# Kernel tuning notes

Hardware: AMD Instinct MI355X
Metric: run time of the kernel (lower is better)

Reference implementation:

```python
import jax, jax.numpy as jnp
import numpy as np

N, E, D, H = 50000, 800000, 128, 8
DH = D // H
EPS = 1e-12


def setup_inputs() -> dict:
    key = jax.random.key(0)
    ks = jax.random.split(key, 12)
    s = 0.02
    return {
        "h": jax.random.normal(ks[0], (N, D), jnp.float32),
        "Wq": jax.random.normal(ks[1], (D, D), jnp.float32) * s,
        "bq": jax.random.normal(ks[2], (D,), jnp.float32) * s,
        "Wk": jax.random.normal(ks[3], (D, D), jnp.float32) * s,
        "bk": jax.random.normal(ks[4], (D,), jnp.float32) * s,
        "Wv": jax.random.normal(ks[5], (D, D), jnp.float32) * s,
        "bv": jax.random.normal(ks[6], (D,), jnp.float32) * s,
        "Wo": jax.random.normal(ks[7], (D, D), jnp.float32) * s,
        "bo": jax.random.normal(ks[8], (D,), jnp.float32) * s,
        "gamma": jnp.ones((D,), jnp.float32),
        "beta": jnp.zeros((D,), jnp.float32),
        "src": jax.random.randint(ks[9], (E,), 0, N, jnp.int32),
        "dst": jax.random.randint(ks[10], (E,), 0, N, jnp.int32),
    }


def reference(h, Wq, bq, Wk, bk, Wv, bv, Wo, bo, gamma, beta, src, dst):
    n = h.shape[0]
    # node-wise projections, split into heads: [N, H, DH]
    Q = (h @ Wq + bq).reshape(n, H, DH)
    K = (h @ Wk + bk).reshape(n, H, DH)
    V = (h @ Wv + bv).reshape(n, H, DH)
    # edge-wise scores: sum over head dim of K[src] * Q[dst] -> [E, H]
    scores = jnp.sum(K[src] * Q[dst], axis=-1)
    # edge softmax, normalized over incoming edges of each dst node
    m = jax.lax.stop_gradient(jax.ops.segment_max(scores, dst, num_segments=n))
    ex = jnp.exp(scores - m[dst])
    denom = jax.ops.segment_sum(ex, dst, num_segments=n)
    p = ex / denom[dst]  # [E, H]
    # weighted message + scatter-sum aggregate -> [N, H, DH]
    msg = V[src] * p[:, :, None]
    agg = jax.ops.segment_sum(msg, dst, num_segments=n).reshape(n, D)
    # BertSelfOutput: dense + residual + layernorm (dropout is identity in eval)
    y = agg @ Wo + bo + h
    mu = jnp.mean(y, axis=-1, keepdims=True)
    var = jnp.mean(jnp.square(y - mu), axis=-1, keepdims=True)
    out = (y - mu) / jnp.sqrt(var + EPS) * gamma + beta
    return out
```

## Files before the change

### kernel.cpp

```cpp
#include <hip/hip_runtime.h>
#include <hip/hip_bf16.h>
#include <math.h>

#define D 128
#define EPS 1e-12f
#define CPAD 16

typedef __attribute__((ext_vector_type(8))) short bf16x8;
typedef __attribute__((ext_vector_type(4))) float f32x4;
typedef __attribute__((ext_vector_type(2))) float f32x2;

__device__ __forceinline__ unsigned short f2bf(float f) {
    unsigned int u = __float_as_uint(f);
    return (unsigned short)((u + 0x7fffu + ((u >> 16) & 1u)) >> 16);
}
__device__ __forceinline__ float bf2f_lo(unsigned int packed) {
    return __uint_as_float(packed << 16);
}
__device__ __forceinline__ float bf2f_hi(unsigned int packed) {
    return __uint_as_float(packed & 0xffff0000u);
}
__device__ __forceinline__ unsigned char f2fp8(float f) {
    return (unsigned char)__builtin_amdgcn_cvt_pk_fp8_f32(f, f, 0, false);
}

__global__ __launch_bounds__(256) void prep_kernel(
    const float* __restrict__ Wq, const float* __restrict__ Wk,
    const float* __restrict__ Wv, const float* __restrict__ Wo,
    unsigned short* __restrict__ WT,
    const int* __restrict__ dst, int* __restrict__ counts,
    int* __restrict__ ticket, int E) {
    int bx = blockIdx.x;
    int tid = threadIdx.x;
    if (bx < 64) {
        __shared__ unsigned short tile[32][33];
        int m = bx >> 4;
        int t = bx & 15;
        const float* W = (m == 0) ? Wq : (m == 1) ? Wk : (m == 2) ? Wv : Wo;
        int r0 = (t & 3) * 32;
        int c0 = (t >> 2) * 32;
        int row = tid >> 3, c4 = (tid & 7) * 4;
        float4 v = *(const float4*)&W[(size_t)(r0 + row) * D + c0 + c4];
        tile[c4 + 0][row] = f2bf(v.x);
        tile[c4 + 1][row] = f2bf(v.y);
        tile[c4 + 2][row] = f2bf(v.z);
        tile[c4 + 3][row] = f2bf(v.w);
        __syncthreads();
        unsigned int lo = (unsigned int)tile[row][c4] | ((unsigned int)tile[row][c4 + 1] << 16);
        unsigned int hi = (unsigned int)tile[row][c4 + 2] | ((unsigned int)tile[row][c4 + 3] << 16);
        uint2 pk; pk.x = lo; pk.y = hi;
        int n = c0 + row;
        int ct = n >> 4, l15 = n & 15;
        int ks = t & 3;
        int quad = c4 >> 3;
        int j = c4 & 7;
        size_t off = (size_t)m * 16384 + (size_t)(((ct * 4 + ks) * 64) + quad * 16 + l15) * 8 + j;
        *(uint2*)&WT[off] = pk;
    } else {
        int e = ((bx - 64) * 256 + tid) * 4;
        if (e >= E) return;
        if (e + 3 < E) {
            int4 d4 = *(const int4*)&dst[e];
            int4 t4;
            t4.x = atomicAdd(&counts[d4.x * CPAD], 1);
            t4.y = atomicAdd(&counts[d4.y * CPAD], 1);
            t4.z = atomicAdd(&counts[d4.z * CPAD], 1);
            t4.w = atomicAdd(&counts[d4.w * CPAD], 1);
            *(int4*)&ticket[e] = t4;
        } else {
            for (int i = e; i < E; ++i) ticket[i] = atomicAdd(&counts[dst[i] * CPAD], 1);
        }
    }
}

__device__ __forceinline__ int block_incl_scan256(int v, int tid, int* wsum) {
    int lane = tid & 63;
    int wid = tid >> 6;
#pragma unroll
    for (int off = 1; off < 64; off <<= 1) {
        int t = __shfl_up(v, off, 64);
        if (lane >= off) v += t;
    }
    if (lane == 63) wsum[wid] = v;
    __syncthreads();
#pragma unroll
    for (int w = 0; w < 4; ++w)
        if (w < wid) v += wsum[w];
    return v;
}

__global__ void scan1_kernel(const int* __restrict__ counts, int* __restrict__ offsets,
                             int* __restrict__ chunksum, int n) {
    __shared__ int wsum[4];
    int tid = threadIdx.x;
    int i = blockIdx.x * 256 + tid;
    int v = (i < n) ? counts[i * CPAD] : 0;
    int incl = block_incl_scan256(v, tid, wsum);
    if (i < n) offsets[i + 1] = incl;
    if (tid == 255) chunksum[blockIdx.x] = incl;
}

__global__ void scan23_kernel(int* __restrict__ offsets, const int* __restrict__ chunksum, int n) {
    __shared__ int wsum[4];
    int bx = blockIdx.x, tid = threadIdx.x;
    int v = 0;
    for (int t = tid; t < bx; t += 256) v += chunksum[t];
#pragma unroll
    for (int off = 32; off >= 1; off >>= 1) v += __shfl_xor(v, off, 64);
    if ((tid & 63) == 0) wsum[tid >> 6] = v;
    __syncthreads();
    int base = wsum[0] + wsum[1] + wsum[2] + wsum[3];
    int i = bx * 256 + tid;
    if (i < n) {
        offsets[i + 1] += base;
        if (i == 0) offsets[0] = 0;
    }
}

__global__ __launch_bounds__(256) void fill_qkv_kernel(
    const int* __restrict__ dst, const int* __restrict__ src,
    const int* __restrict__ ticket, const int* __restrict__ offsets,
    int* __restrict__ psrc, int E, int e4blocks,
    const float* __restrict__ h, const unsigned short* __restrict__ WT,
    const float* __restrict__ bq, const float* __restrict__ bk, const float* __restrict__ bv,
    unsigned short* __restrict__ Qb, unsigned char* __restrict__ KV8, int n) {
    __shared__ __align__(16) unsigned short wt[16384];
    int bx = blockIdx.x;
    int tid = threadIdx.x;
    if (bx < e4blocks) {
        int e = (bx * 256 + tid) * 4;
        if (e >= E) return;
        if (e + 3 < E) {
            int4 d4 = *(const int4*)&dst[e];
            int4 s4 = *(const int4*)&src[e];
            int4 t4 = *(const int4*)&ticket[e];
            psrc[offsets[d4.x] + t4.x] = s4.x;
            psrc[offsets[d4.y] + t4.y] = s4.y;
            psrc[offsets[d4.z] + t4.z] = s4.z;
            psrc[offsets[d4.w] + t4.w] = s4.w;
        } else {
            for (int i = e; i < E; ++i) psrc[offsets[dst[i]] + ticket[i]] = src[i];
        }
        return;
    }
    int bid = bx - e4blocks;
    int lane = tid & 63, wave = tid >> 6;
    int quad = lane >> 4, l15 = lane & 15;
    int rt = bid * 64 + wave * 16;

    int rowA = min(rt + l15, n - 1);
    bf16x8 af[4];
#pragma unroll
    for (int ks = 0; ks < 4; ++ks) {
        const float* ap = &h[(size_t)rowA * D + ks * 32 + quad * 8];
        float4 a0 = *(const float4*)ap;
        float4 a1 = *(const float4*)(ap + 4);
        union { unsigned short u[8]; bf16x8 v; } pk;
        pk.u[0] = f2bf(a0.x); pk.u[1] = f2bf(a0.y);
        pk.u[2] = f2bf(a0.z); pk.u[3] = f2bf(a0.w);
        pk.u[4] = f2bf(a1.x); pk.u[5] = f2bf(a1.y);
        pk.u[6] = f2bf(a1.z); pk.u[7] = f2bf(a1.w);
        af[ks] = pk.v;
    }

    for (int m = 0; m < 3; ++m) {
#pragma unroll
        for (int it = 0; it < 8; ++it) {
            int idx = it * 256 + tid;
            *(uint4*)&wt[idx * 8] = *(const uint4*)&WT[(size_t)m * 16384 + idx * 8];
        }
        __syncthreads();

        f32x4 acc[8];
#pragma unroll
        for (int ct = 0; ct < 8; ++ct) {
            acc[ct] = (f32x4){0.f, 0.f, 0.f, 0.f};
#pragma unroll
            for (int ks = 0; ks < 4; ++ks) {
                bf16x8 bfr = *(const bf16x8*)&wt[((ct * 4 + ks) * 64 + lane) * 8];
                acc[ct] = __builtin_amdgcn_mfma_f32_16x16x32_bf16(af[ks], bfr, acc[ct], 0, 0, 0);
            }
        }
        __syncthreads();

        const float* bias = (m == 0) ? bq : (m == 1) ? bk : bv;
#pragma unroll
        for (int ct = 0; ct < 8; ++ct) {
            int col = ct * 16 + l15;
            float bb = bias[col];
#pragma unroll
            for (int r = 0; r < 4; ++r) {
                int row = rt + quad * 4 + r;
                if (row < n) {
                    float v = acc[ct][r] + bb;
                    if (m == 0)      Qb[(size_t)row * D + col] = f2bf(v);
                    else if (m == 1) KV8[(size_t)row * 256 + col] = f2fp8(v);
                    else             KV8[(size_t)row * 256 + 128 + col] = f2fp8(v);
                }
            }
        }
    }
}

__global__ __launch_bounds__(256) void edge_attn_kernel(
    const unsigned short* __restrict__ Qb, const unsigned char* __restrict__ KV8,
    const int* __restrict__ offsets, const int* __restrict__ psrc,
    unsigned short* __restrict__ aggb, int n) {
    int node = (blockIdx.x * 256 + threadIdx.x) >> 5;
    int l32 = threadIdx.x & 31;
    if (node >= n) return;
    int start = offsets[node], end = offsets[node + 1];
    int j = l32 >> 3, hd = l32 & 7;

    const unsigned short* qp = &Qb[(size_t)node * D + hd * 16];
    uint4 qa = *(const uint4*)qp;
    uint4 qb = *(const uint4*)(qp + 8);
    float q[16];
    q[0] = bf2f_lo(qa.x);  q[1] = bf2f_hi(qa.x);
    q[2] = bf2f_lo(qa.y);  q[3] = bf2f_hi(qa.y);
    q[4] = bf2f_lo(qa.z);  q[5] = bf2f_hi(qa.z);
    q[6] = bf2f_lo(qa.w);  q[7] = bf2f_hi(qa.w);
    q[8] = bf2f_lo(qb.x);  q[9] = bf2f_hi(qb.x);
    q[10] = bf2f_lo(qb.y); q[11] = bf2f_hi(qb.y);
    q[12] = bf2f_lo(qb.z); q[13] = bf2f_hi(qb.z);
    q[14] = bf2f_lo(qb.w); q[15] = bf2f_hi(qb.w);

    float l = 0.f;
    float acc[16] = {};

    if (start < end) {
        int s0 = psrc[min(start + j, end - 1)];
        int s1 = (start + 4 < end) ? psrc[min(start + 4 + j, end - 1)] : 0;
        const unsigned char* kvp = &KV8[(size_t)s0 * 256 + hd * 16];
        uint4 ku = *(const uint4*)kvp;
        uint4 vu = *(const uint4*)(kvp + 128);
        for (int base = start; base < end; base += 4) {
            const unsigned char* kvpn = &KV8[(size_t)s1 * 256 + hd * 16];
            uint4 kun = *(const uint4*)kvpn;
            uint4 vun = *(const uint4*)(kvpn + 128);
            int s2 = (base + 8 < end) ? psrc[min(base + 8 + j, end - 1)] : 0;
            bool valid = (base + j) < end;

            float kf[16], vf[16];
            {
                f32x2 t;
                t = __builtin_amdgcn_cvt_pk_f32_fp8(ku.x, false); kf[0] = t.x;  kf[1] = t.y;
                t = __builtin_amdgcn_cvt_pk_f32_fp8(ku.x, true);  kf[2] = t.x;  kf[3] = t.y;
                t = __builtin_amdgcn_cvt_pk_f32_fp8(ku.y, false); kf[4] = t.x;  kf[5] = t.y;
                t = __builtin_amdgcn_cvt_pk_f32_fp8(ku.y, true);  kf[6] = t.x;  kf[7] = t.y;
                t = __builtin_amdgcn_cvt_pk_f32_fp8(ku.z, false); kf[8] = t.x;  kf[9] = t.y;
                t = __builtin_amdgcn_cvt_pk_f32_fp8(ku.z, true);  kf[10] = t.x; kf[11] = t.y;
                t = __builtin_amdgcn_cvt_pk_f32_fp8(ku.w, false); kf[12] = t.x; kf[13] = t.y;
                t = __builtin_amdgcn_cvt_pk_f32_fp8(ku.w, true);  kf[14] = t.x; kf[15] = t.y;
                t = __builtin_amdgcn_cvt_pk_f32_fp8(vu.x, false); vf[0] = t.x;  vf[1] = t.y;
                t = __builtin_amdgcn_cvt_pk_f32_fp8(vu.x, true);  vf[2] = t.x;  vf[3] = t.y;
                t = __builtin_amdgcn_cvt_pk_f32_fp8(vu.y, false); vf[4] = t.x;  vf[5] = t.y;
                t = __builtin_amdgcn_cvt_pk_f32_fp8(vu.y, true);  vf[6] = t.x;  vf[7] = t.y;
                t = __builtin_amdgcn_cvt_pk_f32_fp8(vu.z, false); vf[8] = t.x;  vf[9] = t.y;
                t = __builtin_amdgcn_cvt_pk_f32_fp8(vu.z, true);  vf[10] = t.x; vf[11] = t.y;
                t = __builtin_amdgcn_cvt_pk_f32_fp8(vu.w, false); vf[12] = t.x; vf[13] = t.y;
                t = __builtin_amdgcn_cvt_pk_f32_fp8(vu.w, true);  vf[14] = t.x; vf[15] = t.y;
            }

            float sc = q[0] * kf[0];
#pragma unroll
            for (int i = 1; i < 16; ++i) sc = fmaf(q[i], kf[i], sc);

            float p = valid ? __expf(sc) : 0.f;
            l += p;
#pragma unroll
            for (int i = 0; i < 16; ++i) acc[i] = fmaf(p, vf[i], acc[i]);
            ku = kun; vu = vun; s1 = s2;
        }
    }

#pragma unroll
    for (int off = 8; off <= 16; off <<= 1) {
        l += __shfl_xor(l, off, 64);
#pragma unroll
        for (int i = 0; i < 16; ++i) acc[i] += __shfl_xor(acc[i], off, 64);
    }
    float inv = (l > 0.f) ? 1.f / l : 0.f;
    if (j == 0) {
        uint4 o0, o1;
        o0.x = (unsigned int)f2bf(acc[0] * inv) | ((unsigned int)f2bf(acc[1] * inv) << 16);
        o0.y = (unsigned int)f2bf(acc[2] * inv) | ((unsigned int)f2bf(acc[3] * inv) << 16);
        o0.z = (unsigned int)f2bf(acc[4] * inv) | ((unsigned int)f2bf(acc[5] * inv) << 16);
        o0.w = (unsigned int)f2bf(acc[6] * inv) | ((unsigned int)f2bf(acc[7] * inv) << 16);
        o1.x = (unsigned int)f2bf(acc[8] * inv) | ((unsigned int)f2bf(acc[9] * inv) << 16);
        o1.y = (unsigned int)f2bf(acc[10] * inv) | ((unsigned int)f2bf(acc[11] * inv) << 16);
        o1.z = (unsigned int)f2bf(acc[12] * inv) | ((unsigned int)f2bf(acc[13] * inv) << 16);
        o1.w = (unsigned int)f2bf(acc[14] * inv) | ((unsigned int)f2bf(acc[15] * inv) << 16);
        unsigned short* op = &aggb[(size_t)node * D + hd * 16];
        *(uint4*)op = o0;
        *(uint4*)(op + 8) = o1;
    }
}

__global__ __launch_bounds__(256) void out_ln_mfma_kernel(
    const unsigned short* __restrict__ aggb, const unsigned short* __restrict__ WTo,
    const float* __restrict__ bo, const float* __restrict__ hres,
    const float* __restrict__ gamma, const float* __restrict__ beta,
    float* __restrict__ out, int n) {
    int tid = threadIdx.x;
    int lane = tid & 63, wave = tid >> 6;
    int quad = lane >> 4, l15 = lane & 15;
    int rt = blockIdx.x * 64 + wave * 16;

    int rowA = min(rt + l15, n - 1);
    bf16x8 af[4];
#pragma unroll
    for (int ks = 0; ks < 4; ++ks)
        af[ks] = *(const bf16x8*)&aggb[(size_t)rowA * D + ks * 32 + quad * 8];

    f32x4 acc[8];
#pragma unroll
    for (int ct = 0; ct < 8; ++ct) {
        acc[ct] = (f32x4){0.f, 0.f, 0.f, 0.f};
#pragma unroll
        for (int ks = 0; ks < 4; ++ks) {
            bf16x8 bfr = *(const bf16x8*)&WTo[(size_t)((ct * 4 + ks) * 64 + lane) * 8];
            acc[ct] = __builtin_amdgcn_mfma_f32_16x16x32_bf16(af[ks], bfr, acc[ct], 0, 0, 0);
        }
    }

    float bb[8], gg[8], be[8];
#pragma unroll
    for (int ct = 0; ct < 8; ++ct) {
        int col = ct * 16 + l15;
        bb[ct] = bo[col];
        gg[ct] = gamma[col];
        be[ct] = beta[col];
    }
#pragma unroll
    for (int ct = 0; ct < 8; ++ct) {
        int col = ct * 16 + l15;
#pragma unroll
        for (int r = 0; r < 4; ++r) {
            int row = rt + quad * 4 + r;
            float hv = (row < n) ? hres[(size_t)row * D + col] : 0.f;
            acc[ct][r] = acc[ct][r] + bb[ct] + hv;
        }
    }

#pragma unroll
    for (int r = 0; r < 4; ++r) {
        float s1 = 0.f, s2 = 0.f;
#pragma unroll
        for (int ct = 0; ct < 8; ++ct) {
            float v = acc[ct][r];
            s1 += v;
            s2 += v * v;
        }
        s1 += __shfl_xor(s1, 1, 64); s2 += __shfl_xor(s2, 1, 64);
        s1 += __shfl_xor(s1, 2, 64); s2 += __shfl_xor(s2, 2, 64);
        s1 += __shfl_xor(s1, 4, 64); s2 += __shfl_xor(s2, 4, 64);
        s1 += __shfl_xor(s1, 8, 64); s2 += __shfl_xor(s2, 8, 64);
        float mu = s1 * (1.f / 128.f);
        float var = s2 * (1.f / 128.f) - mu * mu;
        float rs = rsqrtf(fmaxf(var, 0.f) + EPS);
        int row = rt + quad * 4 + r;
        if (row < n) {
#pragma unroll
            for (int ct = 0; ct < 8; ++ct) {
                int col = ct * 16 + l15;
                out[(size_t)row * D + col] = (acc[ct][r] - mu) * rs * gg[ct] + be[ct];
            }
        }
    }
}

extern "C" void kernel_launch(void* const* d_in, const int* in_sizes, int n_in,
                              void* d_out, int out_size, void* d_ws, size_t ws_size,
                              hipStream_t stream) {
    const float* h     = (const float*)d_in[0];
    const float* Wq    = (const float*)d_in[1];
    const float* bq    = (const float*)d_in[2];
    const float* Wk    = (const float*)d_in[3];
    const float* bk    = (const float*)d_in[4];
    const float* Wv    = (const float*)d_in[5];
    const float* bv    = (const float*)d_in[6];
    const float* Wo    = (const float*)d_in[7];
    const float* bo    = (const float*)d_in[8];
    const float* gamma = (const float*)d_in[9];
    const float* beta  = (const float*)d_in[10];
    const int* src     = (const int*)d_in[11];
    const int* dst     = (const int*)d_in[12];
    float* out = (float*)d_out;

    int N = in_sizes[0] / D;
    int E = in_sizes[11];

    unsigned short* Qb = (unsigned short*)d_ws;
    unsigned short* Ab = Qb + (size_t)N * D;
    unsigned short* WT = Ab + (size_t)N * D;
    unsigned char* KV8 = (unsigned char*)(WT + 4 * D * D);
    int* counts   = (int*)(KV8 + (size_t)N * 256);
    int* offsets  = counts + (size_t)N * CPAD;
    int* chunksum = offsets + (N + 1);
    int* ticket   = chunksum + 256;
    int* psrc     = ticket + E;

    int nchunks = (N + 255) / 256;
    int e4blocks = ((E + 3) / 4 + 255) / 256;
    int nqkv = (N + 63) / 64;

    hipMemsetAsync(counts, 0, (size_t)N * CPAD * sizeof(int), stream);
    prep_kernel<<<64 + e4blocks, 256, 0, stream>>>(Wq, Wk, Wv, Wo, WT, dst, counts, ticket, E);
    scan1_kernel<<<nchunks, 256, 0, stream>>>(counts, offsets, chunksum, N);
    scan23_kernel<<<nchunks, 256, 0, stream>>>(offsets, chunksum, N);
    fill_qkv_kernel<<<e4blocks + nqkv, 256, 0, stream>>>(
        dst, src, ticket, offsets, psrc, E, e4blocks,
        h, WT, bq, bk, bv, Qb, KV8, N);
    edge_attn_kernel<<<(N + 7) / 8, 256, 0, stream>>>(Qb, KV8, offsets, psrc, Ab, N);
    out_ln_mfma_kernel<<<(N + 63) / 64, 256, 0, stream>>>(Ab, WT + 3 * D * D, bo, h, gamma, beta, out, N);
}
```

Baseline: 217.5 us.

## Fuse edge attention with output projection and LayerNorm via shared-memory staging

```diff
diff --git a/kernel.cpp b/kernel.cpp
--- a/kernel.cpp
+++ b/kernel.cpp
@@ -202,125 +202,130 @@
     }
 }
 
-__global__ __launch_bounds__(256) void edge_attn_kernel(
+__global__ __launch_bounds__(256) void attn_out_kernel(
     const unsigned short* __restrict__ Qb, const unsigned char* __restrict__ KV8,
     const int* __restrict__ offsets, const int* __restrict__ psrc,
-    unsigned short* __restrict__ aggb, int n) {
-    int node = (blockIdx.x * 256 + threadIdx.x) >> 5;
-    int l32 = threadIdx.x & 31;
-    if (node >= n) return;
-    int start = offsets[node], end = offsets[node + 1];
+    const unsigned short* __restrict__ WTo, const float* __restrict__ bo,
+    const float* __restrict__ hres, const float* __restrict__ gamma,
+    const float* __restrict__ beta, float* __restrict__ out, int n) {
+    __shared__ __align__(16) unsigned short agg[64 * 128];
+    int tid = threadIdx.x;
+    int nb = blockIdx.x * 64;
+    int grp = tid >> 5, l32 = tid & 31;
     int j = l32 >> 3, hd = l32 & 7;
 
-    const unsigned short* qp = &Qb[(size_t)node * D + hd * 16];
-    uint4 qa = *(const uint4*)qp;
-    uint4 qb = *(const uint4*)(qp + 8);
-    float q[16];
-    q[0] = bf2f_lo(qa.x);  q[1] = bf2f_hi(qa.x);
-    q[2] = bf2f_lo(qa.y);  q[3] = bf2f_hi(qa.y);
-    q[4] = bf2f_lo(qa.z);  q[5] = bf2f_hi(qa.z);
-    q[6] = bf2f_lo(qa.w);  q[7] = bf2f_hi(qa.w);
-    q[8] = bf2f_lo(qb.x);  q[9] = bf2f_hi(qb.x);
-    q[10] = bf2f_lo(qb.y); q[11] = bf2f_hi(qb.y);
-    q[12] = bf2f_lo(qb.z); q[13] = bf2f_hi(qb.z);
-    q[14] = bf2f_lo(qb.w); q[15] = bf2f_hi(qb.w);
-
-    float l = 0.f;
-    float acc[16] = {};
-
-    if (start < end) {
-        int s0 = psrc[min(start + j, end - 1)];
-        int s1 = (start + 4 < end) ? psrc[min(start + 4 + j, end - 1)] : 0;
-        const unsigned char* kvp = &KV8[(size_t)s0 * 256 + hd * 16];
-        uint4 ku = *(const uint4*)kvp;
-        uint4 vu = *(const uint4*)(kvp + 128);
-        for (int base = start; base < end; base += 4) {
-            const unsigned char* kvpn = &KV8[(size_t)s1 * 256 + hd * 16];
-            uint4 kun = *(const uint4*)kvpn;
-            uint4 vun = *(const uint4*)(kvpn + 128);
-            int s2 = (base + 8 < end) ? psrc[min(base + 8 + j, end - 1)] : 0;
-            bool valid = (base + j) < end;
-
-            float kf[16], vf[16];
-            {
-                f32x2 t;
-                t = __builtin_amdgcn_cvt_pk_f32_fp8(ku.x, false); kf[0] = t.x;  kf[1] = t.y;
-                t = __builtin_amdgcn_cvt_pk_f32_fp8(ku.x, true);  kf[2] = t.x;  kf[3] = t.y;
-                t = __builtin_amdgcn_cvt_pk_f32_fp8(ku.y, false); kf[4] = t.x;  kf[5] = t.y;
-                t = __builtin_amdgcn_cvt_pk_f32_fp8(ku.y, true);  kf[6] = t.x;  kf[7] = t.y;
-                t = __builtin_amdgcn_cvt_pk_f32_fp8(ku.z, false); kf[8] = t.x;  kf[9] = t.y;
-                t = __builtin_amdgcn_cvt_pk_f32_fp8(ku.z, true);  kf[10] = t.x; kf[11] = t.y;
-                t = __builtin_amdgcn_cvt_pk_f32_fp8(ku.w, false); kf[12] = t.x; kf[13] = t.y;
-                t = __builtin_amdgcn_cvt_pk_f32_fp8(ku.w, true);  kf[14] = t.x; kf[15] = t.y;
-                t = __builtin_amdgcn_cvt_pk_f32_fp8(vu.x, false); vf[0] = t.x;  vf[1] = t.y;
-                t = __builtin_amdgcn_cvt_pk_f32_fp8(vu.x, true);  vf[2] = t.x;  vf[3] = t.y;
-                t = __builtin_amdgcn_cvt_pk_f32_fp8(vu.y, false); vf[4] = t.x;  vf[5] = t.y;
-                t = __builtin_amdgcn_cvt_pk_f32_fp8(vu.y, true);  vf[6] = t.x;  vf[7] = t.y;
-                t = __builtin_amdgcn_cvt_pk_f32_fp8(vu.z, false); vf[8] = t.x;  vf[9] = t.y;
-                t = __builtin_amdgcn_cvt_pk_f32_fp8(vu.z, true);  vf[10] = t.x; vf[11] = t.y;
-                t = __builtin_amdgcn_cvt_pk_f32_fp8(vu.w, false); vf[12] = t.x; vf[13] = t.y;
-                t = __builtin_amdgcn_cvt_pk_f32_fp8(vu.w, true);  vf[14] = t.x; vf[15] = t.y;
+    for (int sub = 0; sub < 8; ++sub) {
+        int node = nb + grp * 8 + sub;
+        if (node >= n) break;
+        int start = offsets[node], end = offsets[node + 1];
+
+        const unsigned short* qp = &Qb[(size_t)node * D + hd * 16];
+        uint4 qa = *(const uint4*)qp;
+        uint4 qb = *(const uint4*)(qp + 8);
+        float q[16];
+        q[0] = bf2f_lo(qa.x);  q[1] = bf2f_hi(qa.x);
+        q[2] = bf2f_lo(qa.y);  q[3] = bf2f_hi(qa.y);
+        q[4] = bf2f_lo(qa.z);  q[5] = bf2f_hi(qa.z);
+        q[6] = bf2f_lo(qa.w);  q[7] = bf2f_hi(qa.w);
+        q[8] = bf2f_lo(qb.x);  q[9] = bf2f_hi(qb.x);
+        q[10] = bf2f_lo(qb.y); q[11] = bf2f_hi(qb.y);
+        q[12] = bf2f_lo(qb.z); q[13] = bf2f_hi(qb.z);
+        q[14] = bf2f_lo(qb.w); q[15] = bf2f_hi(qb.w);
+
+        float l = 0.f;
+        float acc[16] = {};
+
+        if (start < end) {
+            int s0 = psrc[min(start + j, end - 1)];
+            int s1 = (start + 4 < end) ? psrc[min(start + 4 + j, end - 1)] : 0;
+            const unsigned char* kvp = &KV8[(size_t)s0 * 256 + hd * 16];
+            uint4 ku = *(const uint4*)kvp;
+            uint4 vu = *(const uint4*)(kvp + 128);
+            for (int base = start; base < end; base += 4) {
+                const unsigned char* kvpn = &KV8[(size_t)s1 * 256 + hd * 16];
+                uint4 kun = *(const uint4*)kvpn;
+                uint4 vun = *(const uint4*)(kvpn + 128);
+                int s2 = (base + 8 < end) ? psrc[min(base + 8 + j, end - 1)] : 0;
+                bool valid = (base + j) < end;
+
+                float kf[16], vf[16];
+                {
+                    f32x2 t;
+                    t = __builtin_amdgcn_cvt_pk_f32_fp8(ku.x, false); kf[0] = t.x;  kf[1] = t.y;
+                    t = __builtin_amdgcn_cvt_pk_f32_fp8(ku.x, true);  kf[2] = t.x;  kf[3] = t.y;
+                    t = __builtin_amdgcn_cvt_pk_f32_fp8(ku.y, false); kf[4] = t.x;  kf[5] = t.y;
+                    t = __builtin_amdgcn_cvt_pk_f32_fp8(ku.y, true);  kf[6] = t.x;  kf[7] = t.y;
+                    t = __builtin_amdgcn_cvt_pk_f32_fp8(ku.z, false); kf[8] = t.x;  kf[9] = t.y;
+                    t = __builtin_amdgcn_cvt_pk_f32_fp8(ku.z, true);  kf[10] = t.x; kf[11] = t.y;
+                    t = __builtin_amdgcn_cvt_pk_f32_fp8(ku.w, false); kf[12] = t.x; kf[13] = t.y;
+                    t = __builtin_amdgcn_cvt_pk_f32_fp8(ku.w, true);  kf[14] = t.x; kf[15] = t.y;
+                    t = __builtin_amdgcn_cvt_pk_f32_fp8(vu.x, false); vf[0] = t.x;  vf[1] = t.y;
+                    t = __builtin_amdgcn_cvt_pk_f32_fp8(vu.x, true);  vf[2] = t.x;  vf[3] = t.y;
+                    t = __builtin_amdgcn_cvt_pk_f32_fp8(vu.y, false); vf[4] = t.x;  vf[5] = t.y;
+                    t = __builtin_amdgcn_cvt_pk_f32_fp8(vu.y, true);  vf[6] = t.x;  vf[7] = t.y;
+                    t = __builtin_amdgcn_cvt_pk_f32_fp8(vu.z, false); vf[8] = t.x;  vf[9] = t.y;
+                    t = __builtin_amdgcn_cvt_pk_f32_fp8(vu.z, true);  vf[10] = t.x; vf[11] = t.y;
+                    t = __builtin_amdgcn_cvt_pk_f32_fp8(vu.w, false); vf[12] = t.x; vf[13] = t.y;
+                    t = __builtin_amdgcn_cvt_pk_f32_fp8(vu.w, true);  vf[14] = t.x; vf[15] = t.y;
+                }
+
+                float sc = q[0] * kf[0];
+#pragma unroll
+                for (int i = 1; i < 16; ++i) sc = fmaf(q[i], kf[i], sc);
+
+                float p = valid ? __expf(sc) : 0.f;
+                l += p;
+#pragma unroll
+                for (int i = 0; i < 16; ++i) acc[i] = fmaf(p, vf[i], acc[i]);
+                ku = kun; vu = vun; s1 = s2;
             }
-
-            float sc = q[0] * kf[0];
-#pragma unroll
-            for (int i = 1; i < 16; ++i) sc = fmaf(q[i], kf[i], sc);
-
-            float p = valid ? __expf(sc) : 0.f;
-            l += p;
-#pragma unroll
-            for (int i = 0; i < 16; ++i) acc[i] = fmaf(p, vf[i], acc[i]);
-            ku = kun; vu = vun; s1 = s2;
-        }
-    }
-
-#pragma unroll
-    for (int off = 8; off <= 16; off <<= 1) {
-        l += __shfl_xor(l, off, 64);
-#pragma unroll
-        for (int i = 0; i < 16; ++i) acc[i] += __shfl_xor(acc[i], off, 64);
-    }
-    float inv = (l > 0.f) ? 1.f / l : 0.f;
-    if (j == 0) {
-        uint4 o0, o1;
-        o0.x = (unsigned int)f2bf(acc[0] * inv) | ((unsigned int)f2bf(acc[1] * inv) << 16);
-        o0.y = (unsigned int)f2bf(acc[2] * inv) | ((unsigned int)f2bf(acc[3] * inv) << 16);
-        o0.z = (unsigned int)f2bf(acc[4] * inv) | ((unsigned int)f2bf(acc[5] * inv) << 16);
-        o0.w = (unsigned int)f2bf(acc[6] * inv) | ((unsigned int)f2bf(acc[7] * inv) << 16);
-        o1.x = (unsigned int)f2bf(acc[8] * inv) | ((unsigned int)f2bf(acc[9] * inv) << 16);
-        o1.y = (unsigned int)f2bf(acc[10] * inv) | ((unsigned int)f2bf(acc[11] * inv) << 16);
-        o1.z = (unsigned int)f2bf(acc[12] * inv) | ((unsigned int)f2bf(acc[13] * inv) << 16);
-        o1.w = (unsigned int)f2bf(acc[14] * inv) | ((unsigned int)f2bf(acc[15] * inv) << 16);
-        unsigned short* op = &aggb[(size_t)node * D + hd * 16];
-        *(uint4*)op = o0;
-        *(uint4*)(op + 8) = o1;
-    }
-}
-
-__global__ __launch_bounds__(256) void out_ln_mfma_kernel(
-    const unsigned short* __restrict__ aggb, const unsigned short* __restrict__ WTo,
-    const float* __restrict__ bo, const float* __restrict__ hres,
-    const float* __restrict__ gamma, const float* __restrict__ beta,
-    float* __restrict__ out, int n) {
-    int tid = threadIdx.x;
+        }
+
+#pragma unroll
+        for (int off = 8; off <= 16; off <<= 1) {
+            l += __shfl_xor(l, off, 64);
+#pragma unroll
+            for (int i = 0; i < 16; ++i) acc[i] += __shfl_xor(acc[i], off, 64);
+        }
+        float inv = (l > 0.f) ? 1.f / l : 0.f;
+        if (j == 0) {
+            uint4 o0, o1;
+            o0.x = (unsigned int)f2bf(acc[0] * inv) | ((unsigned int)f2bf(acc[1] * inv) << 16);
+            o0.y = (unsigned int)f2bf(acc[2] * inv) | ((unsigned int)f2bf(acc[3] * inv) << 16);
+            o0.z = (unsigned int)f2bf(acc[4] * inv) | ((unsigned int)f2bf(acc[5] * inv) << 16);
+            o0.w = (unsigned int)f2bf(acc[6] * inv) | ((unsigned int)f2bf(acc[7] * inv) << 16);
+            o1.x = (unsigned int)f2bf(acc[8] * inv) | ((unsigned int)f2bf(acc[9] * inv) << 16);
+            o1.y = (unsigned int)f2bf(acc[10] * inv) | ((unsigned int)f2bf(acc[11] * inv) << 16);
+            o1.z = (unsigned int)f2bf(acc[12] * inv) | ((unsigned int)f2bf(acc[13] * inv) << 16);
+            o1.w = (unsigned int)f2bf(acc[14] * inv) | ((unsigned int)f2bf(acc[15] * inv) << 16);
+            int row = grp * 8 + sub;
+            int swz = (row & 15) << 3;
+            unsigned short* op = &agg[row * 128];
+            *(uint4*)&op[(hd * 16) ^ swz] = o0;
+            *(uint4*)&op[(hd * 16 + 8) ^ swz] = o1;
+        }
+    }
+    __syncthreads();
+
     int lane = tid & 63, wave = tid >> 6;
     int quad = lane >> 4, l15 = lane & 15;
-    int rt = blockIdx.x * 64 + wave * 16;
-
-    int rowA = min(rt + l15, n - 1);
+    int rt = nb + wave * 16;
+
+    int swzA = l15 << 3;
+    const unsigned short* ap = &agg[(wave * 16 + l15) * 128];
     bf16x8 af[4];
 #pragma unroll
     for (int ks = 0; ks < 4; ++ks)
-        af[ks] = *(const bf16x8*)&aggb[(size_t)rowA * D + ks * 32 + quad * 8];
-
-    f32x4 acc[8];
+        af[ks] = *(const bf16x8*)&ap[(ks * 32 + quad * 8) ^ swzA];
+
+    f32x4 acc2[8];
 #pragma unroll
     for (int ct = 0; ct < 8; ++ct) {
-        acc[ct] = (f32x4){0.f, 0.f, 0.f, 0.f};
+        acc2[ct] = (f32x4){0.f, 0.f, 0.f, 0.f};
 #pragma unroll
         for (int ks = 0; ks < 4; ++ks) {
             bf16x8 bfr = *(const bf16x8*)&WTo[(size_t)((ct * 4 + ks) * 64 + lane) * 8];
-            acc[ct] = __builtin_amdgcn_mfma_f32_16x16x32_bf16(af[ks], bfr, acc[ct], 0, 0, 0);
+            acc2[ct] = __builtin_amdgcn_mfma_f32_16x16x32_bf16(af[ks], bfr, acc2[ct], 0, 0, 0);
         }
     }
 
@@ -339,7 +344,7 @@
         for (int r = 0; r < 4; ++r) {
             int row = rt + quad * 4 + r;
             float hv = (row < n) ? hres[(size_t)row * D + col] : 0.f;
-            acc[ct][r] = acc[ct][r] + bb[ct] + hv;
+            acc2[ct][r] = acc2[ct][r] + bb[ct] + hv;
         }
     }
 
@@ -348,7 +353,7 @@
         float s1 = 0.f, s2 = 0.f;
 #pragma unroll
         for (int ct = 0; ct < 8; ++ct) {
-            float v = acc[ct][r];
+            float v = acc2[ct][r];
             s1 += v;
             s2 += v * v;
         }
@@ -364,7 +369,7 @@
 #pragma unroll
             for (int ct = 0; ct < 8; ++ct) {
                 int col = ct * 16 + l15;
-                out[(size_t)row * D + col] = (acc[ct][r] - mu) * rs * gg[ct] + be[ct];
+                out[(size_t)row * D + col] = (acc2[ct][r] - mu) * rs * gg[ct] + be[ct];
             }
         }
     }
@@ -392,8 +397,7 @@
     int E = in_sizes[11];
 
     unsigned short* Qb = (unsigned short*)d_ws;
-    unsigned short* Ab = Qb + (size_t)N * D;
-    unsigned short* WT = Ab + (size_t)N * D;
+    unsigned short* WT = Qb + (size_t)N * D;
     unsigned char* KV8 = (unsigned char*)(WT + 4 * D * D);
     int* counts   = (int*)(KV8 + (size_t)N * 256);
     int* offsets  = counts + (size_t)N * CPAD;
@@ -412,6 +416,6 @@
     fill_qkv_kernel<<<e4blocks + nqkv, 256, 0, stream>>>(
         dst, src, ticket, offsets, psrc, E, e4blocks,
         h, WT, bq, bk, bv, Qb, KV8, N);
-    edge_attn_kernel<<<(N + 7) / 8, 256, 0, stream>>>(Qb, KV8, offsets, psrc, Ab, N);
-    out_ln_mfma_kernel<<<(N + 63) / 64, 256, 0, stream>>>(Ab, WT + 3 * D * D, bo, h, gamma, beta, out, N);
-}
+    attn_out_kernel<<<(N + 63) / 64, 256, 0, stream>>>(
+        Qb, KV8, offsets, psrc, WT + 3 * D * D, bo, h, gamma, beta, out, N);
+}
```

Result: slower. 233.0 us (+7.1%).

## Replace global prefix scan with atomic chunk allocation and int2 node ranges

Applied to the files above, without the earlier changes.

```diff
diff --git a/kernel.cpp b/kernel.cpp
--- a/kernel.cpp
+++ b/kernel.cpp
@@ -89,61 +89,28 @@
     return v;
 }
 
-__global__ void scan1_kernel(const int* __restrict__ counts, int* __restrict__ offsets,
-                             int* __restrict__ chunksum, int n) {
-    __shared__ int wsum[4];
-    int tid = threadIdx.x;
-    int i = blockIdx.x * 256 + tid;
-    int v = (i < n) ? counts[i * CPAD] : 0;
-    int incl = block_incl_scan256(v, tid, wsum);
-    if (i < n) offsets[i + 1] = incl;
-    if (tid == 255) chunksum[blockIdx.x] = incl;
-}
-
-__global__ void scan23_kernel(int* __restrict__ offsets, const int* __restrict__ chunksum, int n) {
-    __shared__ int wsum[4];
-    int bx = blockIdx.x, tid = threadIdx.x;
-    int v = 0;
-    for (int t = tid; t < bx; t += 256) v += chunksum[t];
-#pragma unroll
-    for (int off = 32; off >= 1; off >>= 1) v += __shfl_xor(v, off, 64);
-    if ((tid & 63) == 0) wsum[tid >> 6] = v;
-    __syncthreads();
-    int base = wsum[0] + wsum[1] + wsum[2] + wsum[3];
-    int i = bx * 256 + tid;
-    if (i < n) {
-        offsets[i + 1] += base;
-        if (i == 0) offsets[0] = 0;
-    }
-}
-
-__global__ __launch_bounds__(256) void fill_qkv_kernel(
-    const int* __restrict__ dst, const int* __restrict__ src,
-    const int* __restrict__ ticket, const int* __restrict__ offsets,
-    int* __restrict__ psrc, int E, int e4blocks,
+__global__ __launch_bounds__(256) void alloc_qkv_kernel(
+    const int* __restrict__ counts, int* __restrict__ cursor, int2* __restrict__ off2,
+    int nchunks,
     const float* __restrict__ h, const unsigned short* __restrict__ WT,
     const float* __restrict__ bq, const float* __restrict__ bk, const float* __restrict__ bv,
     unsigned short* __restrict__ Qb, unsigned char* __restrict__ KV8, int n) {
     __shared__ __align__(16) unsigned short wt[16384];
     int bx = blockIdx.x;
     int tid = threadIdx.x;
-    if (bx < e4blocks) {
-        int e = (bx * 256 + tid) * 4;
-        if (e >= E) return;
-        if (e + 3 < E) {
-            int4 d4 = *(const int4*)&dst[e];
-            int4 s4 = *(const int4*)&src[e];
-            int4 t4 = *(const int4*)&ticket[e];
-            psrc[offsets[d4.x] + t4.x] = s4.x;
-            psrc[offsets[d4.y] + t4.y] = s4.y;
-            psrc[offsets[d4.z] + t4.z] = s4.z;
-            psrc[offsets[d4.w] + t4.w] = s4.w;
-        } else {
-            for (int i = e; i < E; ++i) psrc[offsets[dst[i]] + ticket[i]] = src[i];
-        }
+    if (bx < nchunks) {
+        __shared__ int wsum[4];
+        __shared__ int basesh;
+        int i = bx * 256 + tid;
+        int c = (i < n) ? counts[i * CPAD] : 0;
+        int incl = block_incl_scan256(c, tid, wsum);
+        if (tid == 255) basesh = atomicAdd(cursor, incl);
+        __syncthreads();
+        int start = basesh + incl - c;
+        if (i < n) off2[i] = make_int2(start, start + c);
         return;
     }
-    int bid = bx - e4blocks;
+    int bid = bx - nchunks;
     int lane = tid & 63, wave = tid >> 6;
     int quad = lane >> 4, l15 = lane & 15;
     int rt = bid * 64 + wave * 16;
@@ -202,14 +169,34 @@
     }
 }
 
+__global__ __launch_bounds__(256) void scatter_kernel(
+    const int* __restrict__ dst, const int* __restrict__ src,
+    const int* __restrict__ ticket, const int2* __restrict__ off2,
+    int* __restrict__ psrc, int E) {
+    int e = (blockIdx.x * 256 + threadIdx.x) * 4;
+    if (e >= E) return;
+    if (e + 3 < E) {
+        int4 d4 = *(const int4*)&dst[e];
+        int4 s4 = *(const int4*)&src[e];
+        int4 t4 = *(const int4*)&ticket[e];
+        psrc[off2[d4.x].x + t4.x] = s4.x;
+        psrc[off2[d4.y].x + t4.y] = s4.y;
+        psrc[off2[d4.z].x + t4.z] = s4.z;
+        psrc[off2[d4.w].x + t4.w] = s4.w;
+    } else {
+        for (int i = e; i < E; ++i) psrc[off2[dst[i]].x + ticket[i]] = src[i];
+    }
+}
+
 __global__ __launch_bounds__(256) void edge_attn_kernel(
     const unsigned short* __restrict__ Qb, const unsigned char* __restrict__ KV8,
-    const int* __restrict__ offsets, const int* __restrict__ psrc,
+    const int2* __restrict__ off2, const int* __restrict__ psrc,
     unsigned short* __restrict__ aggb, int n) {
     int node = (blockIdx.x * 256 + threadIdx.x) >> 5;
     int l32 = threadIdx.x & 31;
     if (node >= n) return;
-    int start = offsets[node], end = offsets[node + 1];
+    int2 se = off2[node];
+    int start = se.x, end = se.y;
     int j = l32 >> 3, hd = l32 & 7;
 
     const unsigned short* qp = &Qb[(size_t)node * D + hd * 16];
@@ -396,22 +383,20 @@
     unsigned short* WT = Ab + (size_t)N * D;
     unsigned char* KV8 = (unsigned char*)(WT + 4 * D * D);
     int* counts   = (int*)(KV8 + (size_t)N * 256);
-    int* offsets  = counts + (size_t)N * CPAD;
-    int* chunksum = offsets + (N + 1);
-    int* ticket   = chunksum + 256;
+    int* cursor   = counts + (size_t)N * CPAD;
+    int2* off2    = (int2*)(cursor + 16);
+    int* ticket   = (int*)(off2 + N);
     int* psrc     = ticket + E;
 
     int nchunks = (N + 255) / 256;
     int e4blocks = ((E + 3) / 4 + 255) / 256;
     int nqkv = (N + 63) / 64;
 
-    hipMemsetAsync(counts, 0, (size_t)N * CPAD * sizeof(int), stream);
+    hipMemsetAsync(counts, 0, ((size_t)N * CPAD + 16) * sizeof(int), stream);
     prep_kernel<<<64 + e4blocks, 256, 0, stream>>>(Wq, Wk, Wv, Wo, WT, dst, counts, ticket, E);
-    scan1_kernel<<<nchunks, 256, 0, stream>>>(counts, offsets, chunksum, N);
-    scan23_kernel<<<nchunks, 256, 0, stream>>>(offsets, chunksum, N);
-    fill_qkv_kernel<<<e4blocks + nqkv, 256, 0, stream>>>(
-        dst, src, ticket, offsets, psrc, E, e4blocks,
-        h, WT, bq, bk, bv, Qb, KV8, N);
-    edge_attn_kernel<<<(N + 7) / 8, 256, 0, stream>>>(Qb, KV8, offsets, psrc, Ab, N);
+    alloc_qkv_kernel<<<nchunks + nqkv, 256, 0, stream>>>(
+        counts, cursor, off2, nchunks, h, WT, bq, bk, bv, Qb, KV8, N);
+    scatter_kernel<<<e4blocks, 256, 0, stream>>>(dst, src, ticket, off2, psrc, E);
+    edge_attn_kernel<<<(N + 7) / 8, 256, 0, stream>>>(Qb, KV8, off2, psrc, Ab, N);
     out_ln_mfma_kernel<<<(N + 63) / 64, 256, 0, stream>>>(Ab, WT + 3 * D * D, bo, h, gamma, beta, out, N);
 }
```

New measurement: 216.3 us, median of 2. No clear change (-0.5%).
